# Performance work log

Hardware: AMD Instinct MI355X
Metric: run time of the kernel (lower is better)

The kernel has to match this reference:

```python
import jax, jax.numpy as jnp
import numpy as np

HIDDEN = 1024
HEADS = 16
HEAD_DIM = HIDDEN // HEADS


def setup_inputs() -> dict:
    key = jax.random.key(0)
    ks = jax.random.split(key, 9)
    B, S = 4, 2048
    s = 1.0 / np.sqrt(HIDDEN)
    return {
        "inputs": jax.random.normal(ks[0], (B, S, HIDDEN), dtype=jnp.float32),
        "Wq": jax.random.normal(ks[1], (HIDDEN, HIDDEN), dtype=jnp.float32) * s,
        "bq": jnp.zeros((HIDDEN,), dtype=jnp.float32),
        "Wk": jax.random.normal(ks[2], (HIDDEN, HIDDEN), dtype=jnp.float32) * s,
        "bk": jnp.zeros((HIDDEN,), dtype=jnp.float32),
        "Wv": jax.random.normal(ks[3], (HIDDEN, HIDDEN), dtype=jnp.float32) * s,
        "bv": jnp.zeros((HIDDEN,), dtype=jnp.float32),
        "Wp": jax.random.normal(ks[4], (HIDDEN, HIDDEN), dtype=jnp.float32) * s,
        "bp": jnp.zeros((HIDDEN,), dtype=jnp.float32),
        "heads_z": jnp.ones((1, HEADS, 1, 1), dtype=jnp.float32),
        "hidden_z": jnp.ones((HIDDEN,), dtype=jnp.float32),
    }


def _split_heads(x):
    # [B,S,HIDDEN] -> [B,H,S,Dh]
    B, S, _ = x.shape
    return x.reshape(B, S, HEADS, HEAD_DIM).transpose(0, 2, 1, 3)


def reference(inputs, Wq, bq, Wk, bk, Wv, bv, Wp, bp, heads_z, hidden_z):
    q = _split_heads(inputs @ Wq.T + bq)
    k = _split_heads(inputs @ Wk.T + bk)
    v = _split_heads(inputs @ Wv.T + bv)
    scores = jnp.einsum("bhqd,bhkd->bhqk", q, k) / jnp.sqrt(
        jnp.asarray(HEAD_DIM, dtype=q.dtype))
    probs = jax.nn.softmax(scores, axis=-1)
    ctx = jnp.einsum("bhqk,bhkd->bhqd", probs, v)  # [B,H,S,Dh]
    ctx = ctx * heads_z
    B, H, S, D = ctx.shape
    ctx = ctx.transpose(0, 2, 1, 3).reshape(B, S, H * D)
    out = ctx @ Wp.T + bp
    out = out * hidden_z
    return out
```

## Files before the change

kernel.cpp:

```cpp
#include <hip/hip_runtime.h>
#include <hip/hip_bf16.h>

#define HID 1024
#define NH 16
#define DH 64
#define SEQ 2048
#define NB 4
#define MTOT (NB*SEQ)
#define SM_SCALE 0.18033688f

typedef __attribute__((ext_vector_type(4))) float f32x4;
typedef __attribute__((ext_vector_type(16))) float f32x16;
typedef __attribute__((ext_vector_type(8))) __bf16 bf16x8;
typedef __attribute__((ext_vector_type(4))) __bf16 bf16x4;
typedef __attribute__((ext_vector_type(2))) __bf16 bf16x2;
typedef __attribute__((ext_vector_type(2))) int i32x2;

__device__ __forceinline__ f32x4 mfma16(bf16x8 a, bf16x8 b, f32x4 c) {
    return __builtin_amdgcn_mfma_f32_16x16x32_bf16(a, b, c, 0, 0, 0);
}
__device__ __forceinline__ f32x16 mfma32(bf16x8 a, bf16x8 b, f32x16 c) {
    return __builtin_amdgcn_mfma_f32_32x32x16_bf16(a, b, c, 0, 0, 0);
}

__device__ __forceinline__ void gload16(const void* g, void* l) {
    __builtin_amdgcn_global_load_lds(
        (const __attribute__((address_space(1))) unsigned int*)g,
        (__attribute__((address_space(3))) unsigned int*)l, 16, 0, 0);
}

__device__ __forceinline__ float fexp2(float x) {
#if __has_builtin(__builtin_amdgcn_exp2f)
    return __builtin_amdgcn_exp2f(x);
#else
    return exp2f(x);
#endif
}

__device__ __forceinline__ unsigned pkbf2(float lo, float hi) {
    union { bf16x2 v; unsigned u; } c;
    c.v = (bf16x2){ (__bf16)lo, (__bf16)hi };
    return c.u;
}

#define F3(a,b,c) fmaxf(fmaxf((a),(b)),(c))

__device__ __forceinline__ void swap32(unsigned &a, unsigned &b) {
#if __has_builtin(__builtin_amdgcn_permlane32_swap)
    i32x2 r = __builtin_amdgcn_permlane32_swap((int)a, (int)b, false, false);
    a = (unsigned)r.x; b = (unsigned)r.y;
#else
    const bool hi = (threadIdx.x & 32) != 0;
    unsigned ta = __shfl_xor(a, 32), tb = __shfl_xor(b, 32);
    unsigned na = hi ? tb : a;
    unsigned nb = hi ? b : ta;
    a = na; b = nb;
#endif
}

__device__ __forceinline__ float swapmaxf(float x) {
    unsigned a = __float_as_uint(x), b = a;
    swap32(a, b);
    return fmaxf(__uint_as_float(a), __uint_as_float(b));
}

__global__ __launch_bounds__(256)
void cvt5(const float* __restrict__ X,  const float* __restrict__ Wq,
          const float* __restrict__ Wk, const float* __restrict__ Wv,
          const float* __restrict__ Wp,
          __bf16* __restrict__ Xb,  __bf16* __restrict__ Wqb,
          __bf16* __restrict__ Wkb, __bf16* __restrict__ Wvb,
          __bf16* __restrict__ Wpb)
{
    const float* src; __bf16* dst; int n;
    switch (blockIdx.y) {
        case 0:  src = X;  dst = Xb;  n = MTOT * HID; break;
        case 1:  src = Wq; dst = Wqb; n = HID * HID;  break;
        case 2:  src = Wk; dst = Wkb; n = HID * HID;  break;
        case 3:  src = Wv; dst = Wvb; n = HID * HID;  break;
        default: src = Wp; dst = Wpb; n = HID * HID;  break;
    }
    const int stride = gridDim.x * 256 * 4;
    for (int i = (blockIdx.x * 256 + threadIdx.x) * 4; i < n; i += stride) {
        float4 v = *(const float4*)(src + i);
        bf16x4 o = { (__bf16)v.x, (__bf16)v.y, (__bf16)v.z, (__bf16)v.w };
        *(bf16x4*)(dst + i) = o;
    }
}

__global__ __launch_bounds__(256)
void gemm_qkv(const __bf16* __restrict__ A,
              const __bf16* __restrict__ Wq, const __bf16* __restrict__ Wk,
              const __bf16* __restrict__ Wv,
              const float* __restrict__ bq, const float* __restrict__ bk,
              const float* __restrict__ bv,
              __bf16* __restrict__ Qo, __bf16* __restrict__ Ko, __bf16* __restrict__ Vo)
{
    __shared__ __bf16 As[128 * 32];
    __shared__ __bf16 Bs[128 * 32];
    const int mode = blockIdx.z;
    const __bf16* W    = mode == 0 ? Wq : mode == 1 ? Wk : Wv;
    const float*  bias = mode == 0 ? bq : mode == 1 ? bk : bv;

    const int tid  = threadIdx.x;
    const int lane = tid & 63, wid = tid >> 6;
    const int m0 = blockIdx.x * 128;
    const int n0 = blockIdx.y * 128;
    const int wm = (wid >> 1) * 64, wn = (wid & 1) * 64;

    f32x4 acc[4][4];
    #pragma unroll
    for (int i = 0; i < 4; i++)
        #pragma unroll
        for (int j = 0; j < 4; j++) acc[i][j] = (f32x4){0.f, 0.f, 0.f, 0.f};

    for (int kt = 0; kt < HID; kt += 32) {
        #pragma unroll
        for (int i = 0; i < 2; i++) {
            int c = wid * 128 + i * 64 + lane;
            int row = c >> 2, slot = c & 3;
            int ss = slot ^ (row & 3);
            gload16(A + (size_t)(m0 + row) * HID + kt + ss * 8, (char*)As + c * 16);
            gload16(W + (size_t)(n0 + row) * HID + kt + ss * 8, (char*)Bs + c * 16);
        }
        __syncthreads();

        bf16x8 af[4], bfr[4];
        #pragma unroll
        for (int mi = 0; mi < 4; mi++) {
            int row = wm + mi * 16 + (lane & 15);
            int off = row * 64 + (((lane >> 4) * 16) ^ ((row & 3) << 4));
            af[mi] = *(const bf16x8*)((const char*)As + off);
        }
        #pragma unroll
        for (int ni = 0; ni < 4; ni++) {
            int row = wn + ni * 16 + (lane & 15);
            int off = row * 64 + (((lane >> 4) * 16) ^ ((row & 3) << 4));
            bfr[ni] = *(const bf16x8*)((const char*)Bs + off);
        }
        #pragma unroll
        for (int mi = 0; mi < 4; mi++)
            #pragma unroll
            for (int ni = 0; ni < 4; ni++)
                acc[mi][ni] = mfma16(af[mi], bfr[ni], acc[mi][ni]);
        __syncthreads();
    }

    if (mode == 2) {
        #pragma unroll
        for (int mi = 0; mi < 4; mi++)
            #pragma unroll
            for (int ni = 0; ni < 4; ni++) {
                int m = m0 + wm + mi * 16 + ((lane >> 4) * 4);
                int n = n0 + wn + ni * 16 + (lane & 15);
                int b = m >> 11, s = m & (SEQ - 1);
                int h = n >> 6,  d = n & 63;
                bf16x4 o;
                #pragma unroll
                for (int r = 0; r < 4; r++) o[r] = (__bf16)(acc[mi][ni][r] + bias[n]);
                *(bf16x4*)(Vo + ((size_t)(b * NH + h) * DH + d) * SEQ + s) = o;
            }
    } else {
        const float qs = (mode == 0) ? SM_SCALE : 1.0f;
        __bf16* Og = (mode == 0) ? Qo : Ko;
        #pragma unroll
        for (int mi = 0; mi < 4; mi++)
            #pragma unroll
            for (int ni = 0; ni < 4; ni++)
                #pragma unroll
                for (int r = 0; r < 4; r++) {
                    int m = m0 + wm + mi * 16 + ((lane >> 4) * 4) + r;
                    int n = n0 + wn + ni * 16 + (lane & 15);
                    float v = (acc[mi][ni][r] + bias[n]) * qs;
                    int b = m >> 11, s = m & (SEQ - 1);
                    int h = n >> 6,  d = n & 63;
                    Og[((size_t)(b * NH + h) * SEQ + s) * DH + d] = (__bf16)v;
                }
    }
}

__global__ __launch_bounds__(256)
void gemm_proj(const __bf16* __restrict__ A, const __bf16* __restrict__ W,
               const float* __restrict__ bias, const float* __restrict__ hz,
               float* __restrict__ outp)
{
    __shared__ __bf16 As[128 * 32];
    __shared__ __bf16 Bs[128 * 32];
    const int tid  = threadIdx.x;
    const int lane = tid & 63, wid = tid >> 6;
    const int m0 = blockIdx.x * 128;
    const int n0 = blockIdx.y * 128;
    const int wm = (wid >> 1) * 64, wn = (wid & 1) * 64;

    f32x4 acc[4][4];
    #pragma unroll
    for (int i = 0; i < 4; i++)
        #pragma unroll
        for (int j = 0; j < 4; j++) acc[i][j] = (f32x4){0.f, 0.f, 0.f, 0.f};

    for (int kt = 0; kt < HID; kt += 32) {
        #pragma unroll
        for (int i = 0; i < 2; i++) {
            int c = wid * 128 + i * 64 + lane;
            int row = c >> 2, slot = c & 3;
            int ss = slot ^ (row & 3);
            gload16(A + (size_t)(m0 + row) * HID + kt + ss * 8, (char*)As + c * 16);
            gload16(W + (size_t)(n0 + row) * HID + kt + ss * 8, (char*)Bs + c * 16);
        }
        __syncthreads();

        bf16x8 af[4], bfr[4];
        #pragma unroll
        for (int mi = 0; mi < 4; mi++) {
            int row = wm + mi * 16 + (lane & 15);
            int off = row * 64 + (((lane >> 4) * 16) ^ ((row & 3) << 4));
            af[mi] = *(const bf16x8*)((const char*)As + off);
        }
        #pragma unroll
        for (int ni = 0; ni < 4; ni++) {
            int row = wn + ni * 16 + (lane & 15);
            int off = row * 64 + (((lane >> 4) * 16) ^ ((row & 3) << 4));
            bfr[ni] = *(const bf16x8*)((const char*)Bs + off);
        }
        #pragma unroll
        for (int mi = 0; mi < 4; mi++)
            #pragma unroll
            for (int ni = 0; ni < 4; ni++)
                acc[mi][ni] = mfma16(af[mi], bfr[ni], acc[mi][ni]);
        __syncthreads();
    }

    #pragma unroll
    for (int mi = 0; mi < 4; mi++)
        #pragma unroll
        for (int ni = 0; ni < 4; ni++)
            #pragma unroll
            for (int r = 0; r < 4; r++) {
                int m = m0 + wm + mi * 16 + ((lane >> 4) * 4) + r;
                int n = n0 + wn + ni * 16 + (lane & 15);
                outp[(size_t)m * HID + n] = (acc[mi][ni][r] + bias[n]) * hz[n];
            }
}

#define KVB 128

__global__ __launch_bounds__(512, 4)
void attn(const __bf16* __restrict__ Q, const __bf16* __restrict__ K,
          const __bf16* __restrict__ VT, const float* __restrict__ heads_z,
          __bf16* __restrict__ C)
{
    __shared__ __bf16 Ks[2][KVB * 64];
    __shared__ __bf16 Vs[2][64 * KVB];
    const int tid = threadIdx.x, lane = tid & 63, wid = tid >> 6;
    const int lh = lane >> 5;
    const int id = blockIdx.x;
    const int bh = (id & 7) | ((id >> 6) << 3);
    const int qb = (id >> 3) & 7;
    const int b = bh >> 4, hd = bh & 15;
    const __bf16* Qg = Q + (size_t)bh * SEQ * DH;
    const __bf16* Kg = K + (size_t)bh * SEQ * DH;
    const __bf16* Vg = VT + (size_t)bh * DH * SEQ;
    const int q = qb * 256 + wid * 32 + (lane & 31);
    const int r0 = lane & 31;
    const int kx = (r0 & 7) << 4;
    const int vx = (r0 & 15) << 4;

    bf16x8 ones8;
    #pragma unroll
    for (int j = 0; j < 8; j++) ones8[j] = (__bf16)1.0f;

    bf16x8 qf[4];
    #pragma unroll
    for (int s = 0; s < 4; s++)
        qf[s] = *(const bf16x8*)(Qg + (size_t)q * DH + s * 16 + lh * 8);

    f32x16 ctx0, ctx1;
    #pragma unroll
    for (int r = 0; r < 16; r++) { ctx0[r] = 0.f; ctx1[r] = 0.f; }
    float mrun = -1e30f, lrun = 0.f;

    const int kr0 = tid >> 3,          kss0 = (tid & 7) ^ (kr0 & 7);
    const int kr1 = (tid + 512) >> 3,  kss1 = (tid & 7) ^ (kr1 & 7);
    const int vr0 = tid >> 4,          vss0 = (tid & 15) ^ (vr0 & 15);
    const int vr1 = (tid + 512) >> 4,  vss1 = (tid & 15) ^ (vr1 & 15);

    gload16(Kg + (size_t)kr0 * DH + kss0 * 8, (char*)&Ks[0][0] + tid * 16);
    gload16(Kg + (size_t)kr1 * DH + kss1 * 8, (char*)&Ks[0][0] + (tid + 512) * 16);
    gload16(Vg + (size_t)vr0 * SEQ + 0 + vss0 * 8, (char*)&Vs[0][0] + tid * 16);
    gload16(Vg + (size_t)vr1 * SEQ + 0 + vss1 * 8, (char*)&Vs[0][0] + (tid + 512) * 16);
    __syncthreads();

    int cur = 0;
    for (int kv0 = 0; kv0 < SEQ; kv0 += KVB) {
        if (kv0 + KVB < SEQ) {
            int nx = kv0 + KVB;
            gload16(Kg + (size_t)(nx + kr0) * DH + kss0 * 8, (char*)&Ks[cur ^ 1][0] + tid * 16);
            gload16(Kg + (size_t)(nx + kr1) * DH + kss1 * 8, (char*)&Ks[cur ^ 1][0] + (tid + 512) * 16);
            gload16(Vg + (size_t)vr0 * SEQ + nx + vss0 * 8, (char*)&Vs[cur ^ 1][0] + tid * 16);
            gload16(Vg + (size_t)vr1 * SEQ + nx + vss1 * 8, (char*)&Vs[cur ^ 1][0] + (tid + 512) * 16);
        }

        #pragma unroll
        for (int hh = 0; hh < 2; hh++) {
            const char* Kb = (const char*)&Ks[cur][0] + hh * 64 * 128;
            const char* Vb = (const char*)&Vs[cur][0];

            f32x16 st0, st1;
            #pragma unroll
            for (int r = 0; r < 16; r++) { st0[r] = 0.f; st1[r] = 0.f; }
            __builtin_amdgcn_s_setprio(1);
            #pragma unroll
            for (int s = 0; s < 4; s++) {
                int co = (2 * s + lh) << 4;
                bf16x8 k0 = *(const bf16x8*)(Kb + r0 * 128 + (co ^ kx));
                bf16x8 k1 = *(const bf16x8*)(Kb + (r0 + 32) * 128 + (co ^ kx));
                st0 = mfma32(k0, qf[s], st0);
                st1 = mfma32(k1, qf[s], st1);
            }
            __builtin_amdgcn_s_setprio(0);

            float l1[11];
            l1[0] = F3(st0[0],  st0[1],  st0[2]);
            l1[1] = F3(st0[3],  st0[4],  st0[5]);
            l1[2] = F3(st0[6],  st0[7],  st0[8]);
            l1[3] = F3(st0[9],  st0[10], st0[11]);
            l1[4] = F3(st0[12], st0[13], st0[14]);
            l1[5] = F3(st0[15], st1[0],  st1[1]);
            l1[6] = F3(st1[2],  st1[3],  st1[4]);
            l1[7] = F3(st1[5],  st1[6],  st1[7]);
            l1[8] = F3(st1[8],  st1[9],  st1[10]);
            l1[9] = F3(st1[11], st1[12], st1[13]);
            l1[10] = fmaxf(st1[14], st1[15]);
            float l2a = F3(l1[0], l1[1], l1[2]);
            float l2b = F3(l1[3], l1[4], l1[5]);
            float l2c = F3(l1[6], l1[7], l1[8]);
            float l2d = fmaxf(l1[9], l1[10]);
            float pml = F3(F3(l2a, l2b, l2c), l2d, mrun) - 0.f;
            if (!__all(pml <= mrun + 8.f)) {
                float pm = swapmaxf(pml);
                float nm = fmaxf(mrun, pm);
                float al = fexp2(mrun - nm);
                lrun *= al; mrun = nm;
                #pragma unroll
                for (int r = 0; r < 16; r++) { ctx0[r] *= al; ctx1[r] *= al; }
            }
            const float mneg = -mrun;
            #pragma unroll
            for (int r = 0; r < 16; r++) {
                st0[r] = fexp2(st0[r] + mneg);
                st1[r] = fexp2(st1[r] + mneg);
            }

            unsigned X0 = pkbf2(st0[0],  st0[1]),  X1 = pkbf2(st0[2],  st0[3]);
            unsigned X2 = pkbf2(st0[4],  st0[5]),  X3 = pkbf2(st0[6],  st0[7]);
            unsigned X4 = pkbf2(st0[8],  st0[9]),  X5 = pkbf2(st0[10], st0[11]);
            unsigned X6 = pkbf2(st0[12], st0[13]), X7 = pkbf2(st0[14], st0[15]);
            unsigned Y0 = pkbf2(st1[0],  st1[1]),  Y1 = pkbf2(st1[2],  st1[3]);
            unsigned Y2 = pkbf2(st1[4],  st1[5]),  Y3 = pkbf2(st1[6],  st1[7]);
            unsigned Y4 = pkbf2(st1[8],  st1[9]),  Y5 = pkbf2(st1[10], st1[11]);
            unsigned Y6 = pkbf2(st1[12], st1[13]), Y7 = pkbf2(st1[14], st1[15]);
            swap32(X0, X2); swap32(X1, X3);
            swap32(X4, X6); swap32(X5, X7);
            swap32(Y0, Y2); swap32(Y1, Y3);
            swap32(Y4, Y6); swap32(Y5, Y7);
            union W4 { unsigned w[4]; bf16x8 v; };
            W4 pf[4];
            pf[0].w[0]=X0; pf[0].w[1]=X1; pf[0].w[2]=X2; pf[0].w[3]=X3;
            pf[1].w[0]=X4; pf[1].w[1]=X5; pf[1].w[2]=X6; pf[1].w[3]=X7;
            pf[2].w[0]=Y0; pf[2].w[1]=Y1; pf[2].w[2]=Y2; pf[2].w[3]=Y3;
            pf[3].w[0]=Y4; pf[3].w[1]=Y5; pf[3].w[2]=Y6; pf[3].w[3]=Y7;

            st0[0] = 0.f;
            #pragma unroll
            for (int s = 0; s < 4; s++) st0 = mfma32(ones8, pf[s].v, st0);

            __builtin_amdgcn_s_setprio(1);
            #pragma unroll
            for (int s = 0; s < 4; s++) {
                int co = (hh * 8 + 2 * s + lh) << 4;
                bf16x8 v0 = *(const bf16x8*)(Vb + r0 * 256 + (co ^ vx));
                bf16x8 v1 = *(const bf16x8*)(Vb + (r0 + 32) * 256 + (co ^ vx));
                ctx0 = mfma32(v0, pf[s].v, ctx0);
                ctx1 = mfma32(v1, pf[s].v, ctx1);
            }
            __builtin_amdgcn_s_setprio(0);

            lrun += st0[0];
        }

        __syncthreads();
        cur ^= 1;
    }

    const float hzv = heads_z[hd];
    const float rl = hzv / lrun;
    __bf16* Crow = C + (size_t)(b * SEQ + q) * HID + hd * DH;
    #pragma unroll
    for (int g = 0; g < 4; g++) {
        bf16x4 o0, o1;
        #pragma unroll
        for (int j = 0; j < 4; j++) {
            o0[j] = (__bf16)(ctx0[4 * g + j] * rl);
            o1[j] = (__bf16)(ctx1[4 * g + j] * rl);
        }
        int d0 = 8 * g + 4 * lh;
        *(bf16x4*)(Crow + d0) = o0;
        *(bf16x4*)(Crow + 32 + d0) = o1;
    }
}

extern "C" void kernel_launch(void* const* d_in, const int* in_sizes, int n_in,
                              void* d_out, int out_size, void* d_ws, size_t ws_size,
                              hipStream_t stream)
{
    const float* X    = (const float*)d_in[0];
    const float* Wq   = (const float*)d_in[1];
    const float* bq   = (const float*)d_in[2];
    const float* Wk   = (const float*)d_in[3];
    const float* bk   = (const float*)d_in[4];
    const float* Wv   = (const float*)d_in[5];
    const float* bv   = (const float*)d_in[6];
    const float* Wp   = (const float*)d_in[7];
    const float* bp   = (const float*)d_in[8];
    const float* hz   = (const float*)d_in[9];
    const float* hidz = (const float*)d_in[10];

    __bf16* ws  = (__bf16*)d_ws;
    __bf16* Xb  = ws;
    __bf16* Wqb = Xb  + (size_t)MTOT * HID;
    __bf16* Wkb = Wqb + (size_t)HID * HID;
    __bf16* Wvb = Wkb + (size_t)HID * HID;
    __bf16* Wpb = Wvb + (size_t)HID * HID;
    __bf16* Qb  = Wpb + (size_t)HID * HID;
    __bf16* Kb  = Qb  + (size_t)MTOT * HID;
    __bf16* VTb = Kb  + (size_t)MTOT * HID;
    __bf16* Cb  = VTb + (size_t)MTOT * HID;

    cvt5<<<dim3(2048, 5), 256, 0, stream>>>(X, Wq, Wk, Wv, Wp, Xb, Wqb, Wkb, Wvb, Wpb);

    gemm_qkv<<<dim3(MTOT / 128, HID / 128, 3), 256, 0, stream>>>(
        Xb, Wqb, Wkb, Wvb, bq, bk, bv, Qb, Kb, VTb);

    attn<<<dim3(512), 512, 0, stream>>>(Qb, Kb, VTb, hz, Cb);

    gemm_proj<<<dim3(MTOT / 128, HID / 128), 256, 0, stream>>>(Cb, Wpb, bp, hidz, (float*)d_out);
}
```

Measured before the change: 197.2 us.

## Merge two KV half-tiles into one online-softmax step per tile

The attention inner loop now computes QK^T for both 64-row halves of the KV tile before any softmax work. It takes one running-max reduction and one rescale check per 128-key tile instead of per half. The row-sum MFMA with the ones vector is interleaved into the PV MFMA loop so it can overlap with the V loads. This roughly doubles the live score registers (four f32x16 accumulators), which may raise VGPR pressure and cut occupancy.

New measurement: 258.7 us. 31.2% more time.

```diff
diff --git a/kernel.cpp b/kernel.cpp
--- a/kernel.cpp
+++ b/kernel.cpp
@@ -300,93 +300,155 @@
             gload16(Vg + (size_t)vr1 * SEQ + nx + vss1 * 8, (char*)&Vs[cur ^ 1][0] + (tid + 512) * 16);
         }
 
-        #pragma unroll
-        for (int hh = 0; hh < 2; hh++) {
-            const char* Kb = (const char*)&Ks[cur][0] + hh * 64 * 128;
-            const char* Vb = (const char*)&Vs[cur][0];
-
-            f32x16 st0, st1;
-            #pragma unroll
-            for (int r = 0; r < 16; r++) { st0[r] = 0.f; st1[r] = 0.f; }
-            __builtin_amdgcn_s_setprio(1);
-            #pragma unroll
-            for (int s = 0; s < 4; s++) {
-                int co = (2 * s + lh) << 4;
-                bf16x8 k0 = *(const bf16x8*)(Kb + r0 * 128 + (co ^ kx));
-                bf16x8 k1 = *(const bf16x8*)(Kb + (r0 + 32) * 128 + (co ^ kx));
-                st0 = mfma32(k0, qf[s], st0);
-                st1 = mfma32(k1, qf[s], st1);
-            }
-            __builtin_amdgcn_s_setprio(0);
-
-            float l1[11];
-            l1[0] = F3(st0[0],  st0[1],  st0[2]);
-            l1[1] = F3(st0[3],  st0[4],  st0[5]);
-            l1[2] = F3(st0[6],  st0[7],  st0[8]);
-            l1[3] = F3(st0[9],  st0[10], st0[11]);
-            l1[4] = F3(st0[12], st0[13], st0[14]);
-            l1[5] = F3(st0[15], st1[0],  st1[1]);
-            l1[6] = F3(st1[2],  st1[3],  st1[4]);
-            l1[7] = F3(st1[5],  st1[6],  st1[7]);
-            l1[8] = F3(st1[8],  st1[9],  st1[10]);
-            l1[9] = F3(st1[11], st1[12], st1[13]);
-            l1[10] = fmaxf(st1[14], st1[15]);
-            float l2a = F3(l1[0], l1[1], l1[2]);
-            float l2b = F3(l1[3], l1[4], l1[5]);
-            float l2c = F3(l1[6], l1[7], l1[8]);
-            float l2d = fmaxf(l1[9], l1[10]);
-            float pml = F3(F3(l2a, l2b, l2c), l2d, mrun) - 0.f;
-            if (!__all(pml <= mrun + 8.f)) {
-                float pm = swapmaxf(pml);
-                float nm = fmaxf(mrun, pm);
-                float al = fexp2(mrun - nm);
-                lrun *= al; mrun = nm;
-                #pragma unroll
-                for (int r = 0; r < 16; r++) { ctx0[r] *= al; ctx1[r] *= al; }
-            }
-            const float mneg = -mrun;
-            #pragma unroll
-            for (int r = 0; r < 16; r++) {
-                st0[r] = fexp2(st0[r] + mneg);
-                st1[r] = fexp2(st1[r] + mneg);
-            }
-
-            unsigned X0 = pkbf2(st0[0],  st0[1]),  X1 = pkbf2(st0[2],  st0[3]);
-            unsigned X2 = pkbf2(st0[4],  st0[5]),  X3 = pkbf2(st0[6],  st0[7]);
-            unsigned X4 = pkbf2(st0[8],  st0[9]),  X5 = pkbf2(st0[10], st0[11]);
-            unsigned X6 = pkbf2(st0[12], st0[13]), X7 = pkbf2(st0[14], st0[15]);
-            unsigned Y0 = pkbf2(st1[0],  st1[1]),  Y1 = pkbf2(st1[2],  st1[3]);
-            unsigned Y2 = pkbf2(st1[4],  st1[5]),  Y3 = pkbf2(st1[6],  st1[7]);
-            unsigned Y4 = pkbf2(st1[8],  st1[9]),  Y5 = pkbf2(st1[10], st1[11]);
-            unsigned Y6 = pkbf2(st1[12], st1[13]), Y7 = pkbf2(st1[14], st1[15]);
+        const char* Kb0 = (const char*)&Ks[cur][0];
+        const char* Kb1 = Kb0 + 64 * 128;
+        const char* Vb  = (const char*)&Vs[cur][0];
+
+        f32x16 stA0, stA1;
+        #pragma unroll
+        for (int r = 0; r < 16; r++) { stA0[r] = 0.f; stA1[r] = 0.f; }
+        __builtin_amdgcn_s_setprio(1);
+        #pragma unroll
+        for (int s = 0; s < 4; s++) {
+            int co = (2 * s + lh) << 4;
+            bf16x8 k0 = *(const bf16x8*)(Kb0 + r0 * 128 + (co ^ kx));
+            bf16x8 k1 = *(const bf16x8*)(Kb0 + (r0 + 32) * 128 + (co ^ kx));
+            stA0 = mfma32(k0, qf[s], stA0);
+            stA1 = mfma32(k1, qf[s], stA1);
+        }
+        __builtin_amdgcn_s_setprio(0);
+
+        f32x16 stB0, stB1;
+        #pragma unroll
+        for (int r = 0; r < 16; r++) { stB0[r] = 0.f; stB1[r] = 0.f; }
+        __builtin_amdgcn_s_setprio(1);
+        #pragma unroll
+        for (int s = 0; s < 4; s++) {
+            int co = (2 * s + lh) << 4;
+            bf16x8 k0 = *(const bf16x8*)(Kb1 + r0 * 128 + (co ^ kx));
+            bf16x8 k1 = *(const bf16x8*)(Kb1 + (r0 + 32) * 128 + (co ^ kx));
+            stB0 = mfma32(k0, qf[s], stB0);
+            stB1 = mfma32(k1, qf[s], stB1);
+        }
+        __builtin_amdgcn_s_setprio(0);
+
+        float l1[11];
+        l1[0]  = F3(stA0[0],  stA0[1],  stA0[2]);
+        l1[1]  = F3(stA0[3],  stA0[4],  stA0[5]);
+        l1[2]  = F3(stA0[6],  stA0[7],  stA0[8]);
+        l1[3]  = F3(stA0[9],  stA0[10], stA0[11]);
+        l1[4]  = F3(stA0[12], stA0[13], stA0[14]);
+        l1[5]  = F3(stA0[15], stA1[0],  stA1[1]);
+        l1[6]  = F3(stA1[2],  stA1[3],  stA1[4]);
+        l1[7]  = F3(stA1[5],  stA1[6],  stA1[7]);
+        l1[8]  = F3(stA1[8],  stA1[9],  stA1[10]);
+        l1[9]  = F3(stA1[11], stA1[12], stA1[13]);
+        l1[10] = fmaxf(stA1[14], stA1[15]);
+        float m1[11];
+        m1[0]  = F3(stB0[0],  stB0[1],  stB0[2]);
+        m1[1]  = F3(stB0[3],  stB0[4],  stB0[5]);
+        m1[2]  = F3(stB0[6],  stB0[7],  stB0[8]);
+        m1[3]  = F3(stB0[9],  stB0[10], stB0[11]);
+        m1[4]  = F3(stB0[12], stB0[13], stB0[14]);
+        m1[5]  = F3(stB0[15], stB1[0],  stB1[1]);
+        m1[6]  = F3(stB1[2],  stB1[3],  stB1[4]);
+        m1[7]  = F3(stB1[5],  stB1[6],  stB1[7]);
+        m1[8]  = F3(stB1[8],  stB1[9],  stB1[10]);
+        m1[9]  = F3(stB1[11], stB1[12], stB1[13]);
+        m1[10] = fmaxf(stB1[14], stB1[15]);
+        float a2 = F3(F3(l1[0], l1[1], l1[2]), F3(l1[3], l1[4], l1[5]), F3(l1[6], l1[7], l1[8]));
+        float b2 = F3(F3(m1[0], m1[1], m1[2]), F3(m1[3], m1[4], m1[5]), F3(m1[6], m1[7], m1[8]));
+        float c2 = F3(F3(l1[9], l1[10], m1[9]), m1[10], mrun);
+        float pml = F3(a2, b2, c2);
+        if (!__all(pml <= mrun + 8.f)) {
+            float pm = swapmaxf(pml);
+            float nm = fmaxf(mrun, pm);
+            float al = fexp2(mrun - nm);
+            lrun *= al; mrun = nm;
+            #pragma unroll
+            for (int r = 0; r < 16; r++) { ctx0[r] *= al; ctx1[r] *= al; }
+        }
+        const float mneg = -mrun;
+
+        union W4 { unsigned w[4]; bf16x8 v; };
+
+        #pragma unroll
+        for (int r = 0; r < 16; r++) {
+            stA0[r] = fexp2(stA0[r] + mneg);
+            stA1[r] = fexp2(stA1[r] + mneg);
+        }
+        {
+            unsigned X0 = pkbf2(stA0[0],  stA0[1]),  X1 = pkbf2(stA0[2],  stA0[3]);
+            unsigned X2 = pkbf2(stA0[4],  stA0[5]),  X3 = pkbf2(stA0[6],  stA0[7]);
+            unsigned X4 = pkbf2(stA0[8],  stA0[9]),  X5 = pkbf2(stA0[10], stA0[11]);
+            unsigned X6 = pkbf2(stA0[12], stA0[13]), X7 = pkbf2(stA0[14], stA0[15]);
+            unsigned Y0 = pkbf2(stA1[0],  stA1[1]),  Y1 = pkbf2(stA1[2],  stA1[3]);
+            unsigned Y2 = pkbf2(stA1[4],  stA1[5]),  Y3 = pkbf2(stA1[6],  stA1[7]);
+            unsigned Y4 = pkbf2(stA1[8],  stA1[9]),  Y5 = pkbf2(stA1[10], stA1[11]);
+            unsigned Y6 = pkbf2(stA1[12], stA1[13]), Y7 = pkbf2(stA1[14], stA1[15]);
             swap32(X0, X2); swap32(X1, X3);
             swap32(X4, X6); swap32(X5, X7);
             swap32(Y0, Y2); swap32(Y1, Y3);
             swap32(Y4, Y6); swap32(Y5, Y7);
-            union W4 { unsigned w[4]; bf16x8 v; };
             W4 pf[4];
             pf[0].w[0]=X0; pf[0].w[1]=X1; pf[0].w[2]=X2; pf[0].w[3]=X3;
             pf[1].w[0]=X4; pf[1].w[1]=X5; pf[1].w[2]=X6; pf[1].w[3]=X7;
             pf[2].w[0]=Y0; pf[2].w[1]=Y1; pf[2].w[2]=Y2; pf[2].w[3]=Y3;
             pf[3].w[0]=Y4; pf[3].w[1]=Y5; pf[3].w[2]=Y6; pf[3].w[3]=Y7;
 
-            st0[0] = 0.f;
-            #pragma unroll
-            for (int s = 0; s < 4; s++) st0 = mfma32(ones8, pf[s].v, st0);
-
+            stA0[0] = 0.f;
             __builtin_amdgcn_s_setprio(1);
             #pragma unroll
             for (int s = 0; s < 4; s++) {
-                int co = (hh * 8 + 2 * s + lh) << 4;
+                int co = (2 * s + lh) << 4;
                 bf16x8 v0 = *(const bf16x8*)(Vb + r0 * 256 + (co ^ vx));
                 bf16x8 v1 = *(const bf16x8*)(Vb + (r0 + 32) * 256 + (co ^ vx));
+                stA0 = mfma32(ones8, pf[s].v, stA0);
                 ctx0 = mfma32(v0, pf[s].v, ctx0);
                 ctx1 = mfma32(v1, pf[s].v, ctx1);
             }
             __builtin_amdgcn_s_setprio(0);
-
-            lrun += st0[0];
-        }
+        }
+
+        #pragma unroll
+        for (int r = 0; r < 16; r++) {
+            stB0[r] = fexp2(stB0[r] + mneg);
+            stB1[r] = fexp2(stB1[r] + mneg);
+        }
+        {
+            unsigned X0 = pkbf2(stB0[0],  stB0[1]),  X1 = pkbf2(stB0[2],  stB0[3]);
+            unsigned X2 = pkbf2(stB0[4],  stB0[5]),  X3 = pkbf2(stB0[6],  stB0[7]);
+            unsigned X4 = pkbf2(stB0[8],  stB0[9]),  X5 = pkbf2(stB0[10], stB0[11]);
+            unsigned X6 = pkbf2(stB0[12], stB0[13]), X7 = pkbf2(stB0[14], stB0[15]);
+            unsigned Y0 = pkbf2(stB1[0],  stB1[1]),  Y1 = pkbf2(stB1[2],  stB1[3]);
+            unsigned Y2 = pkbf2(stB1[4],  stB1[5]),  Y3 = pkbf2(stB1[6],  stB1[7]);
+            unsigned Y4 = pkbf2(stB1[8],  stB1[9]),  Y5 = pkbf2(stB1[10], stB1[11]);
+            unsigned Y6 = pkbf2(stB1[12], stB1[13]), Y7 = pkbf2(stB1[14], stB1[15]);
+            swap32(X0, X2); swap32(X1, X3);
+            swap32(X4, X6); swap32(X5, X7);
+            swap32(Y0, Y2); swap32(Y1, Y3);
+            swap32(Y4, Y6); swap32(Y5, Y7);
+            W4 pf[4];
+            pf[0].w[0]=X0; pf[0].w[1]=X1; pf[0].w[2]=X2; pf[0].w[3]=X3;
+            pf[1].w[0]=X4; pf[1].w[1]=X5; pf[1].w[2]=X6; pf[1].w[3]=X7;
+            pf[2].w[0]=Y0; pf[2].w[1]=Y1; pf[2].w[2]=Y2; pf[2].w[3]=Y3;
+            pf[3].w[0]=Y4; pf[3].w[1]=Y5; pf[3].w[2]=Y6; pf[3].w[3]=Y7;
+
+            stB0[0] = 0.f;
+            __builtin_amdgcn_s_setprio(1);
+            #pragma unroll
+            for (int s = 0; s < 4; s++) {
+                int co = (8 + 2 * s + lh) << 4;
+                bf16x8 v0 = *(const bf16x8*)(Vb + r0 * 256 + (co ^ vx));
+                bf16x8 v1 = *(const bf16x8*)(Vb + (r0 + 32) * 256 + (co ^ vx));
+                stB0 = mfma32(ones8, pf[s].v, stB0);
+                ctx0 = mfma32(v0, pf[s].v, ctx0);
+                ctx1 = mfma32(v1, pf[s].v, ctx1);
+            }
+            __builtin_amdgcn_s_setprio(0);
+        }
+
+        lrun += stA0[0] + stB0[0];
 
         __syncthreads();
         cur ^= 1;
```

## Rewrite QKV and projection GEMMs with 256x128 tiles and triple-buffered async loads

Applied to the files above, without the earlier changes.

Both GEMMs are replaced by one templated kernel that uses 512 threads, 256x128 output tiles, BK=64 and a three-stage LDS ring filled by direct global-to-LDS loads. A and B loads for future stages are interleaved between two MFMA phases, with explicit vmcnt/lgkmcnt waits, raw barriers and priority boosts. The aim is to hide global memory latency and remove the full sync-per-32-K step of the old single-buffered loop. It uses much more LDS (144KB, one block per CU) and depends on hand-tuned wait counts.

After: 195.6 us. No clear change (-0.8%).

```diff
diff --git a/kernel.cpp b/kernel.cpp
--- a/kernel.cpp
+++ b/kernel.cpp
@@ -88,25 +88,40 @@
     }
 }
 
-__global__ __launch_bounds__(256)
-void gemm_qkv(const __bf16* __restrict__ A,
-              const __bf16* __restrict__ Wq, const __bf16* __restrict__ Wk,
-              const __bf16* __restrict__ Wv,
-              const float* __restrict__ bq, const float* __restrict__ bk,
-              const float* __restrict__ bv,
-              __bf16* __restrict__ Qo, __bf16* __restrict__ Ko, __bf16* __restrict__ Vo)
+template<int PROJ>
+__global__ __launch_bounds__(512, 1)
+void gemm8(const __bf16* __restrict__ A,
+           const __bf16* __restrict__ Wq, const __bf16* __restrict__ Wk,
+           const __bf16* __restrict__ Wv,
+           const float* __restrict__ bq, const float* __restrict__ bk,
+           const float* __restrict__ bv, const float* __restrict__ hz,
+           __bf16* __restrict__ Qo, __bf16* __restrict__ Ko,
+           __bf16* __restrict__ Vo, float* __restrict__ Po)
 {
-    __shared__ __bf16 As[128 * 32];
-    __shared__ __bf16 Bs[128 * 32];
-    const int mode = blockIdx.z;
-    const __bf16* W    = mode == 0 ? Wq : mode == 1 ? Wk : Wv;
-    const float*  bias = mode == 0 ? bq : mode == 1 ? bk : bv;
-
-    const int tid  = threadIdx.x;
-    const int lane = tid & 63, wid = tid >> 6;
-    const int m0 = blockIdx.x * 128;
-    const int n0 = blockIdx.y * 128;
-    const int wm = (wid >> 1) * 64, wn = (wid & 1) * 64;
+    __shared__ __bf16 As[3][256 * 64];
+    __shared__ __bf16 Bs[3][128 * 64];
+    const int tid = threadIdx.x, lane = tid & 63, wid = tid >> 6;
+    const int m0 = blockIdx.x * 256, n0 = blockIdx.y * 128;
+    const int wr = wid >> 1, wc = wid & 1;
+    const int mode = PROJ ? 3 : (int)blockIdx.z;
+
+    const __bf16* W    = PROJ ? Wq : (mode == 0 ? Wq : mode == 1 ? Wk : Wv);
+    const float*  bias = PROJ ? bq : (mode == 0 ? bq : mode == 1 ? bk : bv);
+
+    const int cA0 = tid, cA1 = tid + 512, cA2 = tid + 1024, cA3 = tid + 1536;
+    const int cB0 = tid, cB1 = tid + 512;
+    const __bf16* aA0 = A + (size_t)(m0 + (cA0 >> 3)) * HID + ((cA0 & 7) ^ ((cA0 >> 3) & 7)) * 8;
+    const __bf16* aA1 = A + (size_t)(m0 + (cA1 >> 3)) * HID + ((cA1 & 7) ^ ((cA1 >> 3) & 7)) * 8;
+    const __bf16* aA2 = A + (size_t)(m0 + (cA2 >> 3)) * HID + ((cA2 & 7) ^ ((cA2 >> 3) & 7)) * 8;
+    const __bf16* aA3 = A + (size_t)(m0 + (cA3 >> 3)) * HID + ((cA3 & 7) ^ ((cA3 >> 3) & 7)) * 8;
+    const __bf16* bB0 = W + (size_t)(n0 + (cB0 >> 3)) * HID + ((cB0 & 7) ^ ((cB0 >> 3) & 7)) * 8;
+    const __bf16* bB1 = W + (size_t)(n0 + (cB1 >> 3)) * HID + ((cB1 & 7) ^ ((cB1 >> 3) & 7)) * 8;
+
+#define STAGE_A(sl, j) do { char* d_ = (char*)&As[sl][0]; int kk_ = (j) * 64; \
+    gload16(aA0 + kk_, d_ + cA0 * 16); gload16(aA1 + kk_, d_ + cA1 * 16);     \
+    gload16(aA2 + kk_, d_ + cA2 * 16); gload16(aA3 + kk_, d_ + cA3 * 16); } while (0)
+#define STAGE_B(sl, j) do { char* d_ = (char*)&Bs[sl][0]; int kk_ = (j) * 64; \
+    gload16(bB0 + kk_, d_ + cB0 * 16); gload16(bB1 + kk_, d_ + cB1 * 16); } while (0)
 
     f32x4 acc[4][4];
     #pragma unroll
@@ -114,45 +129,102 @@
         #pragma unroll
         for (int j = 0; j < 4; j++) acc[i][j] = (f32x4){0.f, 0.f, 0.f, 0.f};
 
-    for (int kt = 0; kt < HID; kt += 32) {
-        #pragma unroll
-        for (int i = 0; i < 2; i++) {
-            int c = wid * 128 + i * 64 + lane;
-            int row = c >> 2, slot = c & 3;
-            int ss = slot ^ (row & 3);
-            gload16(A + (size_t)(m0 + row) * HID + kt + ss * 8, (char*)As + c * 16);
-            gload16(W + (size_t)(n0 + row) * HID + kt + ss * 8, (char*)Bs + c * 16);
-        }
-        __syncthreads();
-
-        bf16x8 af[4], bfr[4];
-        #pragma unroll
-        for (int mi = 0; mi < 4; mi++) {
-            int row = wm + mi * 16 + (lane & 15);
-            int off = row * 64 + (((lane >> 4) * 16) ^ ((row & 3) << 4));
-            af[mi] = *(const bf16x8*)((const char*)As + off);
-        }
-        #pragma unroll
-        for (int ni = 0; ni < 4; ni++) {
-            int row = wn + ni * 16 + (lane & 15);
-            int off = row * 64 + (((lane >> 4) * 16) ^ ((row & 3) << 4));
-            bfr[ni] = *(const bf16x8*)((const char*)Bs + off);
-        }
+    const int la = lane & 15, lk = lane >> 4;
+
+    STAGE_A(0, 0); STAGE_B(0, 0);
+    STAGE_A(1, 1); STAGE_B(1, 1);
+    asm volatile("s_waitcnt vmcnt(6)" ::: "memory");
+    __builtin_amdgcn_s_barrier();
+
+    int slc = 0;
+    for (int j = 0; j < 16; ++j) {
+        const char* Ab = (const char*)&As[slc][0];
+        const char* Bb = (const char*)&Bs[slc][0];
+        const int js = j + 2;
+        const int sls = slc == 0 ? 2 : slc - 1;
+
+        bf16x8 af[4][2], bf0[2][2];
+        #pragma unroll
+        for (int mi = 0; mi < 4; mi++)
+            #pragma unroll
+            for (int ks = 0; ks < 2; ks++) {
+                int row = wr * 64 + mi * 16 + la;
+                af[mi][ks] = *(const bf16x8*)(Ab + row * 128 +
+                    ((ks * 64 + lk * 16) ^ ((row & 7) << 4)));
+            }
+        #pragma unroll
+        for (int ni = 0; ni < 2; ni++)
+            #pragma unroll
+            for (int ks = 0; ks < 2; ks++) {
+                int row = wc * 64 + ni * 16 + la;
+                bf0[ni][ks] = *(const bf16x8*)(Bb + row * 128 +
+                    ((ks * 64 + lk * 16) ^ ((row & 7) << 4)));
+            }
+        if (js < 16) STAGE_A(sls, js);
+        __builtin_amdgcn_s_barrier();
+        asm volatile("s_waitcnt lgkmcnt(0)" ::: "memory");
+        __builtin_amdgcn_sched_barrier(0);
+        __builtin_amdgcn_s_setprio(1);
+        #pragma unroll
+        for (int mi = 0; mi < 4; mi++)
+            #pragma unroll
+            for (int ni = 0; ni < 2; ni++) {
+                acc[mi][ni] = mfma16(af[mi][0], bf0[ni][0], acc[mi][ni]);
+                acc[mi][ni] = mfma16(af[mi][1], bf0[ni][1], acc[mi][ni]);
+            }
+        __builtin_amdgcn_s_setprio(0);
+        __builtin_amdgcn_s_barrier();
+
+        bf16x8 bf1[2][2];
+        #pragma unroll
+        for (int ni = 0; ni < 2; ni++)
+            #pragma unroll
+            for (int ks = 0; ks < 2; ks++) {
+                int row = wc * 64 + (ni + 2) * 16 + la;
+                bf1[ni][ks] = *(const bf16x8*)(Bb + row * 128 +
+                    ((ks * 64 + lk * 16) ^ ((row & 7) << 4)));
+            }
+        if (js < 16) STAGE_B(sls, js);
+        __builtin_amdgcn_s_barrier();
+        asm volatile("s_waitcnt lgkmcnt(0)" ::: "memory");
+        __builtin_amdgcn_sched_barrier(0);
+        __builtin_amdgcn_s_setprio(1);
+        #pragma unroll
+        for (int mi = 0; mi < 4; mi++)
+            #pragma unroll
+            for (int ni = 0; ni < 2; ni++) {
+                acc[mi][ni + 2] = mfma16(af[mi][0], bf1[ni][0], acc[mi][ni + 2]);
+                acc[mi][ni + 2] = mfma16(af[mi][1], bf1[ni][1], acc[mi][ni + 2]);
+            }
+        __builtin_amdgcn_s_setprio(0);
+
+        if (j < 13)       { asm volatile("s_waitcnt vmcnt(6)" ::: "memory"); }
+        else if (j == 14) { asm volatile("s_waitcnt vmcnt(0)" ::: "memory"); }
+        __builtin_amdgcn_s_barrier();
+
+        slc = slc == 2 ? 0 : slc + 1;
+    }
+#undef STAGE_A
+#undef STAGE_B
+
+    if (PROJ) {
         #pragma unroll
         for (int mi = 0; mi < 4; mi++)
             #pragma unroll
             for (int ni = 0; ni < 4; ni++)
-                acc[mi][ni] = mfma16(af[mi], bfr[ni], acc[mi][ni]);
-        __syncthreads();
-    }
-
-    if (mode == 2) {
+                #pragma unroll
+                for (int r = 0; r < 4; r++) {
+                    int m = m0 + wr * 64 + mi * 16 + lk * 4 + r;
+                    int n = n0 + wc * 64 + ni * 16 + la;
+                    Po[(size_t)m * HID + n] = (acc[mi][ni][r] + bias[n]) * hz[n];
+                }
+    } else if (mode == 2) {
         #pragma unroll
         for (int mi = 0; mi < 4; mi++)
             #pragma unroll
             for (int ni = 0; ni < 4; ni++) {
-                int m = m0 + wm + mi * 16 + ((lane >> 4) * 4);
-                int n = n0 + wn + ni * 16 + (lane & 15);
+                int m = m0 + wr * 64 + mi * 16 + lk * 4;
+                int n = n0 + wc * 64 + ni * 16 + la;
                 int b = m >> 11, s = m & (SEQ - 1);
                 int h = n >> 6,  d = n & 63;
                 bf16x4 o;
@@ -169,77 +241,14 @@
             for (int ni = 0; ni < 4; ni++)
                 #pragma unroll
                 for (int r = 0; r < 4; r++) {
-                    int m = m0 + wm + mi * 16 + ((lane >> 4) * 4) + r;
-                    int n = n0 + wn + ni * 16 + (lane & 15);
+                    int m = m0 + wr * 64 + mi * 16 + lk * 4 + r;
+                    int n = n0 + wc * 64 + ni * 16 + la;
                     float v = (acc[mi][ni][r] + bias[n]) * qs;
                     int b = m >> 11, s = m & (SEQ - 1);
                     int h = n >> 6,  d = n & 63;
                     Og[((size_t)(b * NH + h) * SEQ + s) * DH + d] = (__bf16)v;
                 }
     }
-}
-
-__global__ __launch_bounds__(256)
-void gemm_proj(const __bf16* __restrict__ A, const __bf16* __restrict__ W,
-               const float* __restrict__ bias, const float* __restrict__ hz,
-               float* __restrict__ outp)
-{
-    __shared__ __bf16 As[128 * 32];
-    __shared__ __bf16 Bs[128 * 32];
-    const int tid  = threadIdx.x;
-    const int lane = tid & 63, wid = tid >> 6;
-    const int m0 = blockIdx.x * 128;
-    const int n0 = blockIdx.y * 128;
-    const int wm = (wid >> 1) * 64, wn = (wid & 1) * 64;
-
-    f32x4 acc[4][4];
-    #pragma unroll
-    for (int i = 0; i < 4; i++)
-        #pragma unroll
-        for (int j = 0; j < 4; j++) acc[i][j] = (f32x4){0.f, 0.f, 0.f, 0.f};
-
-    for (int kt = 0; kt < HID; kt += 32) {
-        #pragma unroll
-        for (int i = 0; i < 2; i++) {
-            int c = wid * 128 + i * 64 + lane;
-            int row = c >> 2, slot = c & 3;
-            int ss = slot ^ (row & 3);
-            gload16(A + (size_t)(m0 + row) * HID + kt + ss * 8, (char*)As + c * 16);
-            gload16(W + (size_t)(n0 + row) * HID + kt + ss * 8, (char*)Bs + c * 16);
-        }
-        __syncthreads();
-
-        bf16x8 af[4], bfr[4];
-        #pragma unroll
-        for (int mi = 0; mi < 4; mi++) {
-            int row = wm + mi * 16 + (lane & 15);
-            int off = row * 64 + (((lane >> 4) * 16) ^ ((row & 3) << 4));
-            af[mi] = *(const bf16x8*)((const char*)As + off);
-        }
-        #pragma unroll
-        for (int ni = 0; ni < 4; ni++) {
-            int row = wn + ni * 16 + (lane & 15);
-            int off = row * 64 + (((lane >> 4) * 16) ^ ((row & 3) << 4));
-            bfr[ni] = *(const bf16x8*)((const char*)Bs + off);
-        }
-        #pragma unroll
-        for (int mi = 0; mi < 4; mi++)
-            #pragma unroll
-            for (int ni = 0; ni < 4; ni++)
-                acc[mi][ni] = mfma16(af[mi], bfr[ni], acc[mi][ni]);
-        __syncthreads();
-    }
-
-    #pragma unroll
-    for (int mi = 0; mi < 4; mi++)
-        #pragma unroll
-        for (int ni = 0; ni < 4; ni++)
-            #pragma unroll
-            for (int r = 0; r < 4; r++) {
-                int m = m0 + wm + mi * 16 + ((lane >> 4) * 4) + r;
-                int n = n0 + wn + ni * 16 + (lane & 15);
-                outp[(size_t)m * HID + n] = (acc[mi][ni][r] + bias[n]) * hz[n];
-            }
 }
 
 #define KVB 128
@@ -335,7 +344,7 @@
             float l2b = F3(l1[3], l1[4], l1[5]);
             float l2c = F3(l1[6], l1[7], l1[8]);
             float l2d = fmaxf(l1[9], l1[10]);
-            float pml = F3(F3(l2a, l2b, l2c), l2d, mrun) - 0.f;
+            float pml = F3(F3(l2a, l2b, l2c), l2d, mrun);
             if (!__all(pml <= mrun + 8.f)) {
                 float pm = swapmaxf(pml);
                 float nm = fmaxf(mrun, pm);
@@ -438,10 +447,12 @@
 
     cvt5<<<dim3(2048, 5), 256, 0, stream>>>(X, Wq, Wk, Wv, Wp, Xb, Wqb, Wkb, Wvb, Wpb);
 
-    gemm_qkv<<<dim3(MTOT / 128, HID / 128, 3), 256, 0, stream>>>(
-        Xb, Wqb, Wkb, Wvb, bq, bk, bv, Qb, Kb, VTb);
+    gemm8<0><<<dim3(MTOT / 256, HID / 128, 3), 512, 0, stream>>>(
+        Xb, Wqb, Wkb, Wvb, bq, bk, bv, nullptr, Qb, Kb, VTb, nullptr);
 
     attn<<<dim3(512), 512, 0, stream>>>(Qb, Kb, VTb, hz, Cb);
 
-    gemm_proj<<<dim3(MTOT / 128, HID / 128), 256, 0, stream>>>(Cb, Wpb, bp, hidz, (float*)d_out);
-}
+    gemm8<1><<<dim3(MTOT / 256, HID / 128), 512, 0, stream>>>(
+        Cb, Wpb, nullptr, nullptr, bp, nullptr, nullptr, hidz,
+        nullptr, nullptr, nullptr, (float*)d_out);
+}
```
